# Performance work log

Measured on AMD Instinct MI355X. Metric: run time of the kernel, lower is better.

Reference implementation:

```python
import jax, jax.numpy as jnp
import numpy as np
from jax import lax

B, C, H, W = 8, 128, 64, 64
S = 4          # patch_size
RED = 16       # SE reduction


def setup_inputs() -> dict:
    key = jax.random.key(0)
    ks = jax.random.split(key, 20)
    f = lambda k, shp, s=1.0: jax.random.normal(k, shp, dtype=jnp.float32) * s
    return {
        "F1": f(ks[0], (B, C, H // 2, W // 2)),
        "F2": f(ks[1], (B, C, H, W)),
        "F3": f(ks[2], (B, C, 2 * H, 2 * W)),
        "conv_w": f(ks[3], (3, C, C, 3, 3), 0.02),
        "conv_b": f(ks[4], (3, C), 0.02),
        "qw": f(ks[5], (3, C, C), 0.05), "qb": f(ks[6], (3, C), 0.02),
        "kw": f(ks[7], (3, C, C), 0.05), "kb": f(ks[8], (3, C), 0.02),
        "vw": f(ks[9], (3, C, C), 0.05), "vb": f(ks[10], (3, C), 0.02),
        "ca1_w": f(ks[11], (3 * C // RED, 3 * C), 0.05), "ca1_b": f(ks[12], (3 * C // RED,), 0.02),
        "ca2_w": f(ks[13], (3 * C, 3 * C // RED), 0.05), "ca2_b": f(ks[14], (3 * C,), 0.02),
        "c3d_w": f(ks[15], (C, C, 3), 0.05), "c3d_b": f(ks[16], (C,), 0.02),
        "out_w": f(ks[17], (C, C), 0.05), "out_b": f(ks[18], (C,), 0.02),
    }


def _conv3x3(x, w, b):
    y = lax.conv_general_dilated(x, w, (1, 1), 'SAME',
                                 dimension_numbers=('NCHW', 'OIHW', 'NCHW'))
    return y + b[None, :, None, None]


def _coarse_attn(x, qw, qb, kw, kb, vw, vb):
    # Block-coarse attention; A is block-constant so we never build HWxHW.
    b, c, h, w = x.shape
    hb, wb = h // S, w // S
    xb = x.reshape(b, c, hb, S, wb, S)
    x_avg = xb.mean((3, 5)).reshape(b, c, hb * wb).transpose(0, 2, 1)  # (B, Nb, C)
    Q = x_avg @ qw.T + qb
    K = x_avg @ kw.T + kb
    A = jax.nn.softmax(jnp.einsum('bnc,bmc->bnm', Q, K) / jnp.sqrt(jnp.float32(c)), axis=-1)
    V = x.transpose(0, 2, 3, 1).reshape(b, h * w, c) @ vw.T + vb       # (B, HW, C)
    Vb = V.reshape(b, hb, S, wb, S, c).sum((2, 4)).reshape(b, hb * wb, c)  # block-summed V
    ob = jnp.einsum('bnm,bmc->bnc', A, Vb)                             # (B, Nb, C)
    out = jnp.broadcast_to(ob.reshape(b, hb, 1, wb, 1, c), (b, hb, S, wb, S, c))
    return out.reshape(b, h, w, c).transpose(0, 3, 1, 2)


def reference(F1, F2, F3, conv_w, conv_b, qw, qb, kw, kb, vw, vb,
              ca1_w, ca1_b, ca2_w, ca2_b, c3d_w, c3d_b, out_w, out_b):
    bsz = F2.shape[0]
    # bilinear upsample (align_corners=False == half-pixel == jax.image.resize)
    F1u = jax.image.resize(F1, F2.shape, method='bilinear')
    # adaptive_avg_pool2d 2H,2W -> H,W is exact 2x2 mean pooling
    F3d = F3.reshape(bsz, C, H, 2, W, 2).mean((3, 5))
    ins = [F1u, F2, F3d]
    processed = [
        _conv3x3(ins[i], conv_w[i], conv_b[i])
        + _coarse_attn(ins[i], qw[i], qb[i], kw[i], kb[i], vw[i], vb[i])
        for i in range(3)
    ]
    cat = jnp.concatenate(processed, axis=1)  # (B, 3C, H, W)
    # SE channel attention
    y = cat.mean((2, 3))
    y = jax.nn.sigmoid(jax.nn.relu(y @ ca1_w.T + ca1_b) @ ca2_w.T + ca2_b)
    wf = cat * y[:, :, None, None]
    # conv3d (3,1,1) pad (1,0,0) then take depth index 1 == full contraction over depth
    stack = jnp.stack((wf[:, :C], wf[:, C:2 * C], wf[:, 2 * C:]), axis=2)  # (B, C, 3, H, W)
    mid = jnp.einsum('ocd,bcdhw->bohw', c3d_w, stack) + c3d_b[None, :, None, None]
    return jnp.einsum('oc,bchw->bohw', out_w, mid) + out_b[None, :, None, None]
```

## Files before the change

### kernel.cpp

```cpp
#include <hip/hip_runtime.h>
#include <hip/hip_bf16.h>
#include <cstddef>


typedef __bf16 bf16x8 __attribute__((ext_vector_type(8)));
typedef float f32x4 __attribute__((ext_vector_type(4)));

__device__ __forceinline__ unsigned short f2bf(float f) {
  unsigned int u = __float_as_uint(f);
  return (unsigned short)((u + 0x7fffu + ((u >> 16) & 1u)) >> 16);
}
__device__ __forceinline__ float bf2f(unsigned short h) {
  return __uint_as_float(((unsigned int)h) << 16);
}
__device__ __forceinline__ unsigned int packbf(float a, float b) {
  return (unsigned int)f2bf(a) | ((unsigned int)f2bf(b) << 16);
}

__global__ __launch_bounds__(256) void k_prep0(
    const float* __restrict__ conv_w, unsigned short* __restrict__ WG,
    const float* __restrict__ qw, const float* __restrict__ kw, const float* __restrict__ vw,
    unsigned short* __restrict__ qwB, unsigned short* __restrict__ kwB,
    unsigned short* __restrict__ vwB,
    const float* __restrict__ out_w, const float* __restrict__ c3d_w,
    float* __restrict__ comb2, const float* __restrict__ c3d_b,
    const float* __restrict__ out_b, float* __restrict__ fb,
    unsigned short* __restrict__ INS, float* __restrict__ ym,
    const float* __restrict__ F1, const float* __restrict__ F2,
    const float* __restrict__ F3) {
  int blk = blockIdx.x;
  int t = threadIdx.x;
  __shared__ alignas(16) unsigned short L[64 * 136];
  if (blk < 384) {
    int i = blk >> 7, co = blk & 127;
    float* Lw = (float*)L;
    const float* src = conv_w + (size_t)blk * 1152;
    for (int q = t; q < 1152; q += 256) Lw[q] = src[q];
    __syncthreads();
    for (int id = t; id < 576; id += 256) {
      int tap = id >> 6, cp = id & 63;
      int cc = cp >> 4, e = (cp & 15) * 2;
      unsigned int w = packbf(Lw[(cp * 2) * 9 + tap], Lw[(cp * 2 + 1) * 9 + tap]);
      *(unsigned int*)(WG + ((size_t)(((i * 9 + tap) * 4 + cc) * 128 + co)) * 32 + e) = w;
    }
    return;
  } else if (blk < 576) {
    int idx = (blk - 384) * 256 + t;
    qwB[idx] = f2bf(qw[idx]);
    kwB[idx] = f2bf(kw[idx]);
    vwB[idx] = f2bf(vw[idx]);
    return;
  } else if (blk < 768) {
    int idx = (blk - 576) * 256 + t;
    int j = idx % 384, o = idx / 384;
    int c = j & 127, d = j >> 7;
    float s = 0.f;
    for (int m = 0; m < 128; m++)
      s += out_w[o * 128 + m] * c3d_w[(m * 128 + c) * 3 + d];
    comb2[idx] = s;
    return;
  } else if (blk == 768) {
    if (t < 128) {
      float s = out_b[t];
      for (int m = 0; m < 128; m++) s += out_w[t * 128 + m] * c3d_b[m];
      fb[t] = s;
    }
    for (int z = t; z < 3072; z += 256) ym[z] = 0.f;
    return;
  } else if (blk < 793) {
    int ib = blk - 769;
    uint4 z = {0u, 0u, 0u, 0u};
    for (int id = t; id < 4160; id += 256) {
      int pxI = id >> 4, seg = id & 15;
      int yy, xxp;
      if (pxI < 66) { yy = 0; xxp = pxI; }
      else if (pxI < 132) { yy = 65; xxp = pxI - 66; }
      else if (pxI < 196) { yy = pxI - 131; xxp = 0; }
      else { yy = pxI - 195; xxp = 65; }
      *(uint4*)(INS + (((size_t)ib * 66 + yy) * 66 + xxp) * 128 + seg * 8) = z;
    }
    return;
  }
  int pidx = blk - 793;
  int y = pidx & 63, b = (pidx >> 6) & 7, i = pidx >> 9;
  int ib = i * 8 + b;
  if (i == 1) {
    int x = t & 63, cg = t >> 6;
    unsigned short* lrow = L + x * 136 + cg * 32;
    const float* src = F2 + (((size_t)b * 128 + cg * 32) * 64 + y) * 64 + x;
#pragma unroll 4
    for (int k = 0; k < 32; k += 2) {
      float a = src[(size_t)k * 4096];
      float c = src[(size_t)(k + 1) * 4096];
      *(unsigned int*)(lrow + k) = packbf(a, c);
    }
  } else if (i == 2) {
    int xp = t & 31, cg8 = t >> 5;
    const float* src = F3 + (((size_t)b * 128 + cg8 * 16) * 128 + 2 * y) * 128 + 4 * xp;
    unsigned short* l0 = L + (2 * xp) * 136 + cg8 * 16;
    unsigned short* l1 = L + (2 * xp + 1) * 136 + cg8 * 16;
#pragma unroll
    for (int k = 0; k < 16; ++k) {
      const float* p = src + (size_t)k * 16384;
      float4 a = *(const float4*)p;
      float4 c = *(const float4*)(p + 128);
      l0[k] = f2bf(0.25f * (a.x + a.y + c.x + c.y));
      l1[k] = f2bf(0.25f * (a.z + a.w + c.z + c.w));
    }
  } else {
    int x = t & 63, cg = t >> 6;
    unsigned short* lrow = L + x * 136 + cg * 32;
    int ky = y >> 1, kx = x >> 1;
    int y0, y1, x0, x1;
    float wy0, wx0;
    if (y & 1) { y0 = ky; y1 = (ky + 1 < 32) ? ky + 1 : 31; wy0 = 0.75f; }
    else       { y0 = (ky - 1 > 0) ? ky - 1 : 0; y1 = ky;   wy0 = 0.25f; }
    if (x & 1) { x0 = kx; x1 = (kx + 1 < 32) ? kx + 1 : 31; wx0 = 0.75f; }
    else       { x0 = (kx - 1 > 0) ? kx - 1 : 0; x1 = kx;   wx0 = 0.25f; }
    const float* base = F1 + ((size_t)b * 128 + cg * 32) * 1024;
#pragma unroll 4
    for (int k = 0; k < 32; k += 2) {
      float v[2];
#pragma unroll
      for (int kk = 0; kk < 2; ++kk) {
        const float* p = base + (size_t)(k + kk) * 1024;
        float top = wx0 * p[y0 * 32 + x0] + (1.f - wx0) * p[y0 * 32 + x1];
        float bot = wx0 * p[y1 * 32 + x0] + (1.f - wx0) * p[y1 * 32 + x1];
        v[kk] = wy0 * top + (1.f - wy0) * bot;
      }
      *(unsigned int*)(lrow + k) = packbf(v[0], v[1]);
    }
  }
  __syncthreads();
  unsigned short* dst = INS + (((size_t)ib * 66 + (y + 1)) * 66 + 1) * 128;
#pragma unroll
  for (int q = 0; q < 4; ++q) {
    int id = t + 256 * q;
    int xx = id >> 4, cseg = id & 15;
    uint4 v = *(const uint4*)(&L[xx * 136 + cseg * 8]);
    *(uint4*)(dst + (size_t)id * 8) = v;
  }
}

__global__ __launch_bounds__(256) void k_qkv(
    const unsigned short* __restrict__ INS,
    const unsigned short* __restrict__ qwB, const float* __restrict__ qb,
    const unsigned short* __restrict__ kwB, const float* __restrict__ kb,
    const unsigned short* __restrict__ vwB, const float* __restrict__ vb,
    unsigned short* __restrict__ Qb, unsigned short* __restrict__ Km,
    unsigned short* __restrict__ VT) {
  int nc = blockIdx.x, b = blockIdx.y, i = blockIdx.z;
  int ib = i * 8 + b;
  int qbase = nc * 16;
  int t = threadIdx.x;
  __shared__ alignas(16) unsigned short xb[16 * 136];
  {
    int n = t >> 4, cs = t & 15;
    int gn = qbase + n;
    int by = gn >> 4, bx = gn & 15;
    float acc[8];
#pragma unroll
    for (int e = 0; e < 8; ++e) acc[e] = 0.f;
#pragma unroll
    for (int ry = 0; ry < 4; ++ry) {
      int y = by * 4 + ry;
      const unsigned short* row = INS + (((size_t)ib * 66 + y + 1) * 66 + 1) * 128 + cs * 8;
#pragma unroll
      for (int rx = 0; rx < 4; ++rx) {
        int x = bx * 4 + rx;
        uint4 v0 = *(const uint4*)(row + (size_t)x * 128);
        unsigned int u[4] = {v0.x, v0.y, v0.z, v0.w};
#pragma unroll
        for (int q = 0; q < 4; ++q) {
          acc[2 * q] += bf2f((unsigned short)(u[q] & 0xffffu));
          acc[2 * q + 1] += bf2f((unsigned short)(u[q] >> 16));
        }
      }
    }
#pragma unroll
    for (int m = 0; m < 4; ++m)
      *(unsigned int*)(&xb[n * 136 + cs * 8 + 2 * m]) =
          packbf(acc[2 * m] * (1.f / 16.f), acc[2 * m + 1] * (1.f / 16.f));
  }
  __syncthreads();
  int w = t >> 6, l = t & 63;
  int lr = l & 15, lk = (l >> 4) * 8;
  int cbase = w * 32;
  bf16x8 ax[4];
#pragma unroll
  for (int ks = 0; ks < 4; ++ks)
    ax[ks] = *(const bf16x8*)(&xb[lr * 136 + ks * 32 + lk]);

#pragma unroll
  for (int which = 0; which < 3; ++which) {
    const unsigned short* wB = (which == 0) ? qwB : (which == 1) ? kwB : vwB;
    const float* bias = (which == 0) ? qb : (which == 1) ? kb : vb;
    f32x4 acc[2];
    acc[0] = {0.f, 0.f, 0.f, 0.f};
    acc[1] = acc[0];
#pragma unroll
    for (int ks = 0; ks < 4; ++ks)
#pragma unroll
      for (int nt = 0; nt < 2; ++nt) {
        bf16x8 bw = *(const bf16x8*)(wB + ((size_t)(i * 128 + cbase + nt * 16 + lr)) * 128 + ks * 32 + lk);
        acc[nt] = __builtin_amdgcn_mfma_f32_16x16x32_bf16(ax[ks], bw, acc[nt], 0, 0, 0);
      }
#pragma unroll
    for (int nt = 0; nt < 2; ++nt) {
      int c = cbase + nt * 16 + lr;
      float bv = bias[i * 128 + c];
#pragma unroll
      for (int r = 0; r < 4; ++r) {
        int n = (l >> 4) * 4 + r;
        float v = acc[nt][r] + bv;
        if (which == 0)
          Qb[((size_t)(ib * 256 + qbase + n)) * 128 + c] = f2bf(v);
        else if (which == 1)
          Km[((size_t)(ib * 256 + qbase + n)) * 128 + c] = f2bf(v);
        else
          VT[((size_t)(ib * 128 + c)) * 256 + qbase + n] = f2bf(16.f * v);
      }
    }
  }
}

__global__ __launch_bounds__(256) void k_attn(
    const unsigned short* __restrict__ Qb, const unsigned short* __restrict__ K,
    const unsigned short* __restrict__ VT, float* __restrict__ OB) {
  int nc = blockIdx.x, b = blockIdx.y, i = blockIdx.z;
  int ib = i * 8 + b;
  int qbase = nc * 16;
  int t = threadIdx.x;
  int w = t >> 6, l = t & 63;
  int lr = l & 15, lk = (l >> 4) * 8;
  __shared__ float Ss[16 * 260];
  __shared__ alignas(16) unsigned short Pb[16 * 280];

  const float SC = 0.08838834764831845f;
  {
    bf16x8 aq[4];
#pragma unroll
    for (int ks = 0; ks < 4; ++ks)
      aq[ks] = *(const bf16x8*)(Qb + ((size_t)(ib * 256 + qbase + lr)) * 128 + ks * 32 + lk);
    f32x4 acc[4];
#pragma unroll
    for (int nt = 0; nt < 4; ++nt) acc[nt] = {0.f, 0.f, 0.f, 0.f};
#pragma unroll
    for (int ks = 0; ks < 4; ++ks)
#pragma unroll
      for (int nt = 0; nt < 4; ++nt) {
        bf16x8 bk = *(const bf16x8*)(K + ((size_t)(ib * 256 + w * 64 + nt * 16 + lr)) * 128 + ks * 32 + lk);
        acc[nt] = __builtin_amdgcn_mfma_f32_16x16x32_bf16(aq[ks], bk, acc[nt], 0, 0, 0);
      }
#pragma unroll
    for (int nt = 0; nt < 4; ++nt)
#pragma unroll
      for (int r = 0; r < 4; ++r)
        Ss[((l >> 4) * 4 + r) * 260 + w * 64 + nt * 16 + lr] = acc[nt][r] * SC;
  }
  __syncthreads();
  {
    int n = t >> 4, ms = t & 15;
    float vals[16];
    float mx = -1e30f;
#pragma unroll
    for (int j = 0; j < 16; ++j) { vals[j] = Ss[n * 260 + ms + 16 * j]; mx = fmaxf(mx, vals[j]); }
    for (int d = 1; d < 16; d <<= 1) mx = fmaxf(mx, __shfl_xor(mx, d));
    float sum = 0.f;
#pragma unroll
    for (int j = 0; j < 16; ++j) { vals[j] = __expf(vals[j] - mx); sum += vals[j]; }
    for (int d = 1; d < 16; d <<= 1) sum += __shfl_xor(sum, d);
    float inv = 1.f / sum;
#pragma unroll
    for (int j = 0; j < 16; ++j) Pb[n * 280 + ms + 16 * j] = f2bf(vals[j] * inv);
  }
  __syncthreads();
  {
    f32x4 acc[2];
    acc[0] = {0.f, 0.f, 0.f, 0.f};
    acc[1] = acc[0];
#pragma unroll
    for (int ks = 0; ks < 8; ++ks) {
      bf16x8 ap = *(const bf16x8*)(&Pb[lr * 280 + ks * 32 + lk]);
#pragma unroll
      for (int nt = 0; nt < 2; ++nt) {
        bf16x8 bv = *(const bf16x8*)(VT + ((size_t)(ib * 128 + w * 32 + nt * 16 + lr)) * 256 + ks * 32 + lk);
        acc[nt] = __builtin_amdgcn_mfma_f32_16x16x32_bf16(ap, bv, acc[nt], 0, 0, 0);
      }
    }
#pragma unroll
    for (int nt = 0; nt < 2; ++nt)
#pragma unroll
      for (int r = 0; r < 4; ++r) {
        int q = (l >> 4) * 4 + r;
        int ch = w * 32 + nt * 16 + lr;
        OB[((size_t)(ib * 256 + qbase + q)) * 128 + ch] = acc[nt][r];
      }
  }
}

__global__ __launch_bounds__(256) void k_conv(
    const unsigned short* __restrict__ INS, const unsigned short* __restrict__ WG,
    const float* __restrict__ conv_b, const float* __restrict__ OB,
    unsigned short* __restrict__ catT, float* __restrict__ Ysum) {
  int yr = blockIdx.x;
  int yp = ((yr & 7) << 2) | (yr >> 3);
  int y0 = yp * 2;
  int b = blockIdx.y, i = blockIdx.z;
  int ib = i * 8 + b;
  int t = threadIdx.x;
  __shared__ alignas(16) unsigned short smem[17408];
  int w = t >> 6, l = t & 63;
  int lr = l & 15, q4 = l >> 4;

  f32x4 acc[2][2][4];
#pragma unroll
  for (int ro = 0; ro < 2; ++ro)
#pragma unroll
    for (int s = 0; s < 2; s++)
#pragma unroll
      for (int p = 0; p < 4; p++) acc[ro][s][p] = 0.f;

  auto stageX = [&](int h) {
    for (int cI = t; cI < 2112; cI += 256) {
      int seg = cI & 7, rj = cI >> 3;
      int r = rj / 66, j = rj - r * 66;
      uint4 v = *(const uint4*)(INS + (((size_t)ib * 66 + y0 + r) * 66 + j) * 128 + h * 64 + seg * 8);
      *(uint4*)(&smem[(r * 66 + j) * 64 + ((seg ^ (j & 7)) * 8)]) = v;
    }
  };

  const unsigned short* wbase = WG + (size_t)(i * 9) * 4 * 128 * 32 + (w * 32 + lr) * 32 + q4 * 8;
  auto wload = [&](bf16x8* dst, int s) {
    int tap = s % 9, cc = s / 9;
    const unsigned short* wp = wbase + (size_t)(tap * 4 + cc) * 4096;
    dst[0] = *(const bf16x8*)(wp);
    dst[1] = *(const bf16x8*)(wp + 16 * 32);
  };
  bf16x8 wbuf[4][2];
  stageX(0);
  wload(wbuf[0], 0);
  wload(wbuf[1], 1);
  wload(wbuf[2], 2);
  wload(wbuf[3], 3);
  __syncthreads();

#pragma unroll
  for (int s = 0; s < 36; ++s) {
    int tap = s % 9;
    int cc2 = (s / 9) & 1;
    int dy = tap / 3, dx = tap - dy * 3;
    int sid = cc2 * 4 + q4;
#pragma unroll
    for (int ro = 0; ro < 2; ++ro) {
      bf16x8 bfv[4];
#pragma unroll
      for (int p = 0; p < 4; ++p) {
        int j = p * 16 + lr + dx;
        bfv[p] = *(const bf16x8*)(&smem[((dy + ro) * 66 + j) * 64 + ((sid ^ (j & 7)) * 8)]);
      }
#pragma unroll
      for (int sf = 0; sf < 2; ++sf)
#pragma unroll
        for (int p = 0; p < 4; ++p)
          acc[ro][sf][p] = __builtin_amdgcn_mfma_f32_16x16x32_bf16(wbuf[s & 3][sf], bfv[p], acc[ro][sf][p], 0, 0, 0);
    }
    if (s + 4 < 36) wload(wbuf[s & 3], s + 4);
    if (s == 17) {
      __syncthreads();
      stageX(1);
      __syncthreads();
    }
  }
  __syncthreads();

  unsigned short* Tt = smem;
  int cobase[2];
  cobase[0] = w * 32 + q4 * 4;
  cobase[1] = w * 32 + 16 + q4 * 4;
  float cb[2][4], ys[2][4];
#pragma unroll
  for (int sf = 0; sf < 2; ++sf)
#pragma unroll
    for (int q = 0; q < 4; ++q) {
      cb[sf][q] = conv_b[i * 128 + cobase[sf] + q];
      ys[sf][q] = 0.f;
    }
#pragma unroll
  for (int ro = 0; ro < 2; ++ro) {
    int nbase = ((y0 + ro) >> 2) * 16;
#pragma unroll
    for (int sf = 0; sf < 2; ++sf) {
#pragma unroll
      for (int p = 0; p < 4; ++p) {
        int px = p * 16 + lr;
        int n = nbase + (px >> 2);
        float4 obv = *(const float4*)(OB + ((size_t)(ib * 256 + n)) * 128 + cobase[sf]);
        float v0 = acc[ro][sf][p][0] + cb[sf][0] + obv.x;
        float v1 = acc[ro][sf][p][1] + cb[sf][1] + obv.y;
        float v2 = acc[ro][sf][p][2] + cb[sf][2] + obv.z;
        float v3 = acc[ro][sf][p][3] + cb[sf][3] + obv.w;
        ys[sf][0] += v0; ys[sf][1] += v1; ys[sf][2] += v2; ys[sf][3] += v3;
        int ploc = ro * 64 + px;
        *(unsigned int*)(&Tt[ploc * 136 + cobase[sf]]) = packbf(v0, v1);
        *(unsigned int*)(&Tt[ploc * 136 + cobase[sf] + 2]) = packbf(v2, v3);
      }
    }
  }
#pragma unroll
  for (int sf = 0; sf < 2; ++sf)
#pragma unroll
    for (int q = 0; q < 4; ++q) {
      float r = ys[sf][q];
      r += __shfl_xor(r, 1);
      r += __shfl_xor(r, 2);
      r += __shfl_xor(r, 4);
      r += __shfl_xor(r, 8);
      if (lr == 0) atomicAdd(&Ysum[b * 384 + i * 128 + cobase[sf] + q], r);
    }
  __syncthreads();
  for (int c2 = t; c2 < 2048; c2 += 256) {
    int ploc = c2 >> 4, seg = c2 & 15;
    uint4 v = *(const uint4*)(&Tt[ploc * 136 + seg * 8]);
    int yy = y0 + (ploc >> 6), xx = ploc & 63;
    *(uint4*)(catT + (((size_t)b * 4096) + yy * 64 + xx) * 384 + i * 128 + seg * 8) = v;
  }
}

__global__ __launch_bounds__(256) void k_final(
    const float* __restrict__ Ysum,
    const float* __restrict__ ca1_w, const float* __restrict__ ca1_b,
    const float* __restrict__ ca2_w, const float* __restrict__ ca2_b,
    const float* __restrict__ comb2, const unsigned short* __restrict__ catT,
    const float* __restrict__ fb, float* __restrict__ out) {
  int pc = blockIdx.x, b = blockIdx.y;
  int t = threadIdx.x;
  __shared__ alignas(16) unsigned short fsm[20480];
  __shared__ float ysh[384];
  __shared__ float sig[384];
  __shared__ float z1[24];
  unsigned short* Ab0 = fsm;
  unsigned short* Ab1 = fsm + 5120;
  unsigned short* Bb0 = fsm + 10240;
  unsigned short* Bb1 = fsm + 15360;

  int w = t >> 6, l = t & 63;
  int wo = w >> 1, wp = w & 1;
  int lr = l & 15, lk = (l >> 4) * 8;

  for (int j = t; j < 384; j += 256) ysh[j] = Ysum[b * 384 + j] * (1.f / 4096.f);
  __syncthreads();
  if (t < 24) {
    float s = ca1_b[t];
    for (int k = 0; k < 384; k++) s += ca1_w[t * 384 + k] * ysh[k];
    z1[t] = fmaxf(s, 0.f);
  }
  __syncthreads();
  for (int j = t; j < 384; j += 256) {
    float s = ca2_b[j];
#pragma unroll
    for (int k = 0; k < 24; k++) s += ca2_w[j * 24 + k] * z1[k];
    sig[j] = 1.f / (1.f + __expf(-s));
  }
  __syncthreads();

  f32x4 acc[4][4];
#pragma unroll
  for (int s = 0; s < 4; s++)
#pragma unroll
    for (int p = 0; p < 4; p++) acc[s][p] = 0.f;

  auto stageA = [&](unsigned short* Adst, int c) {
#pragma unroll
    for (int q = 0; q < 2; ++q) {
      int id = t + 256 * q;
      int o = id >> 2, seg = id & 3;
      int jb = c * 32 + seg * 8;
      const float* src = comb2 + (size_t)o * 384 + jb;
      float4 a = *(const float4*)src;
      float4 b4 = *(const float4*)(src + 4);
      alignas(16) unsigned short tmp[8];
      tmp[0] = f2bf(a.x * sig[jb + 0]);
      tmp[1] = f2bf(a.y * sig[jb + 1]);
      tmp[2] = f2bf(a.z * sig[jb + 2]);
      tmp[3] = f2bf(a.w * sig[jb + 3]);
      tmp[4] = f2bf(b4.x * sig[jb + 4]);
      tmp[5] = f2bf(b4.y * sig[jb + 5]);
      tmp[6] = f2bf(b4.z * sig[jb + 6]);
      tmp[7] = f2bf(b4.w * sig[jb + 7]);
      *(uint4*)(&Adst[o * 40 + seg * 8]) = *(uint4*)tmp;
    }
  };

  stageA(Ab0, 0);
  for (int q = 0; q < 2; ++q) {
    int id = t + 256 * q;
    int o = id >> 2, seg = id & 3;
    uint4 vb = *(const uint4*)(catT + ((size_t)b * 4096 + pc * 128 + o) * 384 + seg * 8);
    *(uint4*)(&Bb0[o * 40 + seg * 8]) = vb;
  }
  __syncthreads();

  for (int c = 0; c < 12; ++c) {
    unsigned short* Acur = (c & 1) ? Ab1 : Ab0;
    unsigned short* Bcur = (c & 1) ? Bb1 : Bb0;
    unsigned short* Anxt = (c & 1) ? Ab0 : Ab1;
    unsigned short* Bnxt = (c & 1) ? Bb0 : Bb1;
    uint4 bpf[2];
    if (c < 11) {
      stageA(Anxt, c + 1);
#pragma unroll
      for (int q = 0; q < 2; ++q) {
        int id = t + 256 * q;
        int o = id >> 2, seg = id & 3;
        bpf[q] = *(const uint4*)(catT + ((size_t)b * 4096 + pc * 128 + o) * 384 + (c + 1) * 32 + seg * 8);
      }
    }
    {
      bf16x8 af[4], bf_[4];
#pragma unroll
      for (int sf = 0; sf < 4; ++sf)
        af[sf] = *(const bf16x8*)(&Acur[(wo * 64 + sf * 16 + lr) * 40 + lk]);
#pragma unroll
      for (int p = 0; p < 4; ++p)
        bf_[p] = *(const bf16x8*)(&Bcur[(wp * 64 + p * 16 + lr) * 40 + lk]);
#pragma unroll
      for (int sf = 0; sf < 4; ++sf)
#pragma unroll
        for (int p = 0; p < 4; ++p)
          acc[sf][p] = __builtin_amdgcn_mfma_f32_16x16x32_bf16(af[sf], bf_[p], acc[sf][p], 0, 0, 0);
    }
    if (c < 11) {
#pragma unroll
      for (int q = 0; q < 2; ++q) {
        int id = t + 256 * q;
        int o = id >> 2, seg = id & 3;
        *(uint4*)(&Bnxt[o * 40 + seg * 8]) = bpf[q];
      }
    }
    __syncthreads();
  }

#pragma unroll
  for (int sf = 0; sf < 4; ++sf) {
    int obase = wo * 64 + sf * 16 + (l >> 4) * 4;
#pragma unroll
    for (int p = 0; p < 4; ++p) {
      int px = wp * 64 + p * 16 + lr;
#pragma unroll
      for (int q = 0; q < 4; ++q) {
        int o = obase + q;
        out[((size_t)(b * 128 + o)) * 4096 + pc * 128 + px] = acc[sf][p][q] + fb[o];
      }
    }
  }
}

extern "C" void kernel_launch(void* const* d_in, const int* in_sizes, int n_in,
                              void* d_out, int out_size, void* d_ws, size_t ws_size,
                              hipStream_t stream) {
  const float* F1 = (const float*)d_in[0];
  const float* F2 = (const float*)d_in[1];
  const float* F3 = (const float*)d_in[2];
  const float* conv_w = (const float*)d_in[3];
  const float* conv_b = (const float*)d_in[4];
  const float* qw = (const float*)d_in[5];
  const float* qb = (const float*)d_in[6];
  const float* kw = (const float*)d_in[7];
  const float* kb = (const float*)d_in[8];
  const float* vw = (const float*)d_in[9];
  const float* vb = (const float*)d_in[10];
  const float* ca1_w = (const float*)d_in[11];
  const float* ca1_b = (const float*)d_in[12];
  const float* ca2_w = (const float*)d_in[13];
  const float* ca2_b = (const float*)d_in[14];
  const float* c3d_w = (const float*)d_in[15];
  const float* c3d_b = (const float*)d_in[16];
  const float* out_w = (const float*)d_in[17];
  const float* out_b = (const float*)d_in[18];
  float* out = (float*)d_out;

  char* W = (char*)d_ws;
  unsigned short* INS  = (unsigned short*)W;
  unsigned short* CATT = (unsigned short*)(W + 26763264);
  unsigned short* QmB = (unsigned short*)(W + 51929088);
  unsigned short* KmB = (unsigned short*)(W + 55074816);
  unsigned short* VTB = (unsigned short*)(W + 58220544);
  float* OBm   = (float*)(W + 61366272);
  unsigned short* WG = (unsigned short*)(W + 64512000);
  unsigned short* QWB = (unsigned short*)(W + 65396736);
  unsigned short* KWB = (unsigned short*)(W + 65593344);
  unsigned short* VWB = (unsigned short*)(W + 65789952);
  float* COMB2 = (float*)(W + 65986560);
  float* YM    = (float*)(W + 66183168);
  float* FB    = (float*)(W + 66195456);

  k_prep0<<<2329, 256, 0, stream>>>(conv_w, WG, qw, kw, vw, QWB, KWB, VWB,
                                    out_w, c3d_w, COMB2, c3d_b, out_b, FB, INS, YM,
                                    F1, F2, F3);
  k_qkv<<<dim3(16, 8, 3), 256, 0, stream>>>(INS, QWB, qb, KWB, kb, VWB, vb, QmB, KmB, VTB);
  k_attn<<<dim3(16, 8, 3), 256, 0, stream>>>(QmB, KmB, VTB, OBm);
  k_conv<<<dim3(32, 8, 3), 256, 0, stream>>>(INS, WG, conv_b, OBm, CATT, YM);
  k_final<<<dim3(32, 8), 256, 0, stream>>>(YM, ca1_w, ca1_b, ca2_w, ca2_b, COMB2, CATT, FB, out);
}
```

Measured before the change: 116.5 us.

## Remap conv warps to row x 64-channel tiles, widening per-warp output tile

The 3x3 conv kernel's warp work split changes. Before, each of 4 warps computed 32 output channels for both output rows. Now each warp computes 64 output channels for one row: the wave index selects the row and the channel half. Per step each warp loads 4 LDS B fragments instead of 8 and 4 weight fragments instead of 2, so LDS reads per MFMA drop while global weight traffic per warp doubles. The weight prefetch ring shrinks from depth 4 to depth 3 to keep register pressure in check, which shortens the prefetch lead.

Result: slower. 140.0 us (+20.2%).

```diff
diff --git a/kernel.cpp b/kernel.cpp
--- a/kernel.cpp
+++ b/kernel.cpp
@@ -311,15 +311,14 @@
   int t = threadIdx.x;
   __shared__ alignas(16) unsigned short smem[17408];
   int w = t >> 6, l = t & 63;
+  int ro = w & 1, ch = w >> 1;
   int lr = l & 15, q4 = l >> 4;
 
-  f32x4 acc[2][2][4];
-#pragma unroll
-  for (int ro = 0; ro < 2; ++ro)
-#pragma unroll
-    for (int s = 0; s < 2; s++)
-#pragma unroll
-      for (int p = 0; p < 4; p++) acc[ro][s][p] = 0.f;
+  f32x4 acc[4][4];
+#pragma unroll
+  for (int s = 0; s < 4; s++)
+#pragma unroll
+    for (int p = 0; p < 4; p++) acc[s][p] = 0.f;
 
   auto stageX = [&](int h) {
     for (int cI = t; cI < 2112; cI += 256) {
@@ -330,42 +329,39 @@
     }
   };
 
-  const unsigned short* wbase = WG + (size_t)(i * 9) * 4 * 128 * 32 + (w * 32 + lr) * 32 + q4 * 8;
+  const unsigned short* wbase = WG + (size_t)(i * 9) * 4 * 128 * 32 + (ch * 64 + lr) * 32 + q4 * 8;
   auto wload = [&](bf16x8* dst, int s) {
     int tap = s % 9, cc = s / 9;
     const unsigned short* wp = wbase + (size_t)(tap * 4 + cc) * 4096;
     dst[0] = *(const bf16x8*)(wp);
     dst[1] = *(const bf16x8*)(wp + 16 * 32);
+    dst[2] = *(const bf16x8*)(wp + 32 * 32);
+    dst[3] = *(const bf16x8*)(wp + 48 * 32);
   };
-  bf16x8 wbuf[4][2];
+  bf16x8 wbuf[3][4];
   stageX(0);
   wload(wbuf[0], 0);
   wload(wbuf[1], 1);
-  wload(wbuf[2], 2);
-  wload(wbuf[3], 3);
   __syncthreads();
 
 #pragma unroll
   for (int s = 0; s < 36; ++s) {
+    if (s + 2 < 36) wload(wbuf[(s + 2) % 3], s + 2);
     int tap = s % 9;
     int cc2 = (s / 9) & 1;
     int dy = tap / 3, dx = tap - dy * 3;
     int sid = cc2 * 4 + q4;
-#pragma unroll
-    for (int ro = 0; ro < 2; ++ro) {
-      bf16x8 bfv[4];
-#pragma unroll
-      for (int p = 0; p < 4; ++p) {
-        int j = p * 16 + lr + dx;
-        bfv[p] = *(const bf16x8*)(&smem[((dy + ro) * 66 + j) * 64 + ((sid ^ (j & 7)) * 8)]);
-      }
-#pragma unroll
-      for (int sf = 0; sf < 2; ++sf)
-#pragma unroll
-        for (int p = 0; p < 4; ++p)
-          acc[ro][sf][p] = __builtin_amdgcn_mfma_f32_16x16x32_bf16(wbuf[s & 3][sf], bfv[p], acc[ro][sf][p], 0, 0, 0);
-    }
-    if (s + 4 < 36) wload(wbuf[s & 3], s + 4);
+    bf16x8 bfv[4];
+#pragma unroll
+    for (int p = 0; p < 4; ++p) {
+      int j = p * 16 + lr + dx;
+      bfv[p] = *(const bf16x8*)(&smem[((dy + ro) * 66 + j) * 64 + ((sid ^ (j & 7)) * 8)]);
+    }
+#pragma unroll
+    for (int sf = 0; sf < 4; ++sf)
+#pragma unroll
+      for (int p = 0; p < 4; ++p)
+        acc[sf][p] = __builtin_amdgcn_mfma_f32_16x16x32_bf16(wbuf[s % 3][sf], bfv[p], acc[sf][p], 0, 0, 0);
     if (s == 17) {
       __syncthreads();
       stageX(1);
@@ -375,40 +371,37 @@
   __syncthreads();
 
   unsigned short* Tt = smem;
-  int cobase[2];
-  cobase[0] = w * 32 + q4 * 4;
-  cobase[1] = w * 32 + 16 + q4 * 4;
-  float cb[2][4], ys[2][4];
-#pragma unroll
-  for (int sf = 0; sf < 2; ++sf)
+  int cobase[4];
+#pragma unroll
+  for (int sf = 0; sf < 4; ++sf) cobase[sf] = ch * 64 + sf * 16 + q4 * 4;
+  float cb[4][4], ys[4][4];
+#pragma unroll
+  for (int sf = 0; sf < 4; ++sf)
 #pragma unroll
     for (int q = 0; q < 4; ++q) {
       cb[sf][q] = conv_b[i * 128 + cobase[sf] + q];
       ys[sf][q] = 0.f;
     }
-#pragma unroll
-  for (int ro = 0; ro < 2; ++ro) {
-    int nbase = ((y0 + ro) >> 2) * 16;
-#pragma unroll
-    for (int sf = 0; sf < 2; ++sf) {
-#pragma unroll
-      for (int p = 0; p < 4; ++p) {
-        int px = p * 16 + lr;
-        int n = nbase + (px >> 2);
-        float4 obv = *(const float4*)(OB + ((size_t)(ib * 256 + n)) * 128 + cobase[sf]);
-        float v0 = acc[ro][sf][p][0] + cb[sf][0] + obv.x;
-        float v1 = acc[ro][sf][p][1] + cb[sf][1] + obv.y;
-        float v2 = acc[ro][sf][p][2] + cb[sf][2] + obv.z;
-        float v3 = acc[ro][sf][p][3] + cb[sf][3] + obv.w;
-        ys[sf][0] += v0; ys[sf][1] += v1; ys[sf][2] += v2; ys[sf][3] += v3;
-        int ploc = ro * 64 + px;
-        *(unsigned int*)(&Tt[ploc * 136 + cobase[sf]]) = packbf(v0, v1);
-        *(unsigned int*)(&Tt[ploc * 136 + cobase[sf] + 2]) = packbf(v2, v3);
-      }
-    }
-  }
-#pragma unroll
-  for (int sf = 0; sf < 2; ++sf)
+  int nbase = ((y0 + ro) >> 2) * 16;
+#pragma unroll
+  for (int sf = 0; sf < 4; ++sf) {
+#pragma unroll
+    for (int p = 0; p < 4; ++p) {
+      int px = p * 16 + lr;
+      int n = nbase + (px >> 2);
+      float4 obv = *(const float4*)(OB + ((size_t)(ib * 256 + n)) * 128 + cobase[sf]);
+      float v0 = acc[sf][p][0] + cb[sf][0] + obv.x;
+      float v1 = acc[sf][p][1] + cb[sf][1] + obv.y;
+      float v2 = acc[sf][p][2] + cb[sf][2] + obv.z;
+      float v3 = acc[sf][p][3] + cb[sf][3] + obv.w;
+      ys[sf][0] += v0; ys[sf][1] += v1; ys[sf][2] += v2; ys[sf][3] += v3;
+      int ploc = ro * 64 + px;
+      *(unsigned int*)(&Tt[ploc * 136 + cobase[sf]]) = packbf(v0, v1);
+      *(unsigned int*)(&Tt[ploc * 136 + cobase[sf] + 2]) = packbf(v2, v3);
+    }
+  }
+#pragma unroll
+  for (int sf = 0; sf < 4; ++sf)
 #pragma unroll
     for (int q = 0; q < 4; ++q) {
       float r = ys[sf][q];
```
